# Optimization experiments

Hardware: AMD Instinct MI355X
Metric: run time of the kernel (lower is better)

## Reference

```python
import jax, jax.numpy as jnp
import numpy as np

BN_EPS = 1e-5


def cond_conv(x, att_w, att_b, weight, pad):
    """CondConv: per-sample expert-mixed conv.
    x: [N,C,H,W]; att_w: [K,C]; att_b: [K]; weight: [K,O,I,kh,kw]; pad: (ph,pw)."""
    pooled = x.mean(axis=(2, 3))                         # [N,C]  (AdaptiveAvgPool2d(1))
    att = jax.nn.sigmoid(pooled @ att_w.T + att_b)       # [N,K]  (1x1 conv + sigmoid)
    agg_w = jnp.einsum('nk,koihw->noihw', att, weight)   # per-sample kernels [N,O,I,kh,kw]

    def conv1(xi, wi):
        return jax.lax.conv_general_dilated(
            xi[None], wi, window_strides=(1, 1),
            padding=[(pad[0], pad[0]), (pad[1], pad[1])],
            dimension_numbers=('NCHW', 'OIHW', 'NCHW'))[0]

    return jax.vmap(conv1)(x, agg_w)                     # [N,O,H,W]


def batchnorm(x, gamma, beta):
    # training-mode BN: biased batch stats over (N,H,W)
    mean = x.mean(axis=(0, 2, 3), keepdims=True)
    var = x.var(axis=(0, 2, 3), keepdims=True)
    xn = (x - mean) * jax.lax.rsqrt(var + BN_EPS)
    return xn * gamma[None, :, None, None] + beta[None, :, None, None]


def channel_shuffle(x, g):
    N, C, H, W = x.shape
    return x.reshape(N, g, C // g, H, W).transpose(0, 2, 1, 3, 4).reshape(N, C, H, W)


def setup_inputs() -> dict:
    key = jax.random.key(0)
    ks = jax.random.split(key, 8)
    N, C, H, W = 32, 256, 64, 64
    Cb, K = C // 4, 4
    inp = {
        'x': jax.random.normal(ks[0], (N, C, H, W), jnp.float32),
        'sq_att_w': jax.random.normal(ks[1], (K, Cb), jnp.float32) * 0.1,
        'sq_att_b': jnp.zeros((K,), jnp.float32),
        'sq_w': jax.random.normal(ks[2], (K, Cb, Cb, 3, 3), jnp.float32) * 0.05,
        'sq_g': jnp.ones((Cb,), jnp.float32),
        'sq_b': jnp.zeros((Cb,), jnp.float32),
        'ver_att_w': jax.random.normal(ks[3], (K, Cb), jnp.float32) * 0.1,
        'ver_att_b': jnp.zeros((K,), jnp.float32),
        'ver_w': jax.random.normal(ks[4], (K, Cb, Cb, 3, 1), jnp.float32) * 0.05,
        'ver_g': jnp.ones((Cb,), jnp.float32),
        'ver_b': jnp.zeros((Cb,), jnp.float32),
        'hor_att_w': jax.random.normal(ks[5], (K, Cb), jnp.float32) * 0.1,
        'hor_att_b': jnp.zeros((K,), jnp.float32),
        'hor_w': jax.random.normal(ks[6], (K, Cb, Cb, 1, 3), jnp.float32) * 0.05,
        'hor_g': jnp.ones((Cb,), jnp.float32),
        'hor_b': jnp.zeros((Cb,), jnp.float32),
    }
    return inp


def reference(x, sq_att_w, sq_att_b, sq_w, sq_g, sq_b,
              ver_att_w, ver_att_b, ver_w, ver_g, ver_b,
              hor_att_w, hor_att_b, hor_w, hor_g, hor_b):
    # q_Split: chunk into 4 along channels
    s0, s1, s2, s3 = jnp.split(x, 4, axis=1)
    # square branch: CondConv 3x3 pad 1 + BN
    sq = batchnorm(cond_conv(s1, sq_att_w, sq_att_b, sq_w, (1, 1)), sq_g, sq_b)
    # vertical branch: CondConv 3x1 pad (1,0) + BN (crop layer is Identity since offset=0)
    ve = batchnorm(cond_conv(s2, ver_att_w, ver_att_b, ver_w, (1, 0)), ver_g, ver_b)
    # horizontal branch: CondConv 1x3 pad (0,1) + BN
    ho = batchnorm(cond_conv(s3, hor_att_w, hor_att_b, hor_w, (0, 1)), hor_g, hor_b)
    out = jnp.concatenate((s0, sq, ve, ho), axis=1)
    return channel_shuffle(out, 8)
```

## Files before the change

### kernel.cpp

```cpp
#include <hip/hip_runtime.h>
#include <cstddef>
#include <cstdint>


typedef __attribute__((ext_vector_type(8))) short frag8;
typedef __attribute__((ext_vector_type(16))) float accf16;

#define HW 4096
#define CNT_INV (1.0f / 131072.0f)
#define CSTR 1056
#define RSTR 8448
#define XT_BR (32ull * 66 * 8448)

#define WS_POOLED 0
#define WS_SS     24576
#define WS_PST    24960
#define WS_WBF_SQ  221568
#define WS_WBF_VER 811392
#define WS_WBF_HOR 1008000
#define WS_XT      1204608
#define WS_CVOUT   14586240

__device__ __forceinline__ int shuf_ch(int c) { return ((c & 31) << 3) | (c >> 5); }

__device__ __forceinline__ unsigned bf16pair(float a, float b) {
    unsigned ua = __builtin_bit_cast(unsigned, a);
    unsigned ub = __builtin_bit_cast(unsigned, b);
    ua = (ua + 0x7fffu + ((ua >> 16) & 1u)) >> 16;
    ub = (ub + 0x7fffu + ((ub >> 16) & 1u)) >> 16;
    return ua | (ub << 16);
}

__device__ __forceinline__ unsigned short bf16r(float a) {
    unsigned ua = __builtin_bit_cast(unsigned, a);
    return (unsigned short)((ua + 0x7fffu + ((ua >> 16) & 1u)) >> 16);
}

__device__ __forceinline__ float bf16lo(unsigned u) {
    return __builtin_bit_cast(float, u << 16);
}
__device__ __forceinline__ float bf16hi(unsigned u) {
    return __builtin_bit_cast(float, u & 0xffff0000u);
}

__device__ __forceinline__ void gload_lds16(const void* g, void* l) {
    __builtin_amdgcn_global_load_lds(
        (const __attribute__((address_space(1))) void*)g,
        (__attribute__((address_space(3))) void*)l, 16, 0, 0);
}

__global__ void __launch_bounds__(256) prepass_kernel(
    const float* __restrict__ x, unsigned char* __restrict__ xt,
    float* __restrict__ pooled4) {
    const int bid = blockIdx.x;
    const int hq = bid & 3;
    const int c8 = (bid >> 2) & 7;
    const int n = (bid >> 5) & 31;
    const int b = bid >> 10;
    const int tid = threadIdx.x;
    const int w = tid & 63, q = tid >> 6;
    const float* xb = x + (size_t)(n * 256 + 64 * (b + 1) + c8 * 8) * HW;
    unsigned char* xtb = xt + (size_t)b * XT_BR + (size_t)n * 66 * RSTR + c8 * CSTR;

    float ps[8] = {0.f, 0.f, 0.f, 0.f, 0.f, 0.f, 0.f, 0.f};
#pragma unroll
    for (int it = 0; it < 4; ++it) {
        const int h = hq * 16 + it * 4 + q;
        float v[8];
#pragma unroll
        for (int j = 0; j < 8; ++j) v[j] = xb[(size_t)j * HW + h * 64 + w];
        unsigned pk[4];
#pragma unroll
        for (int j = 0; j < 4; ++j) pk[j] = bf16pair(v[2 * j], v[2 * j + 1]);
        *(uint4*)(xtb + (size_t)(h + 1) * RSTR + (w + 1) * 16) = *(uint4*)pk;
#pragma unroll
        for (int j = 0; j < 8; ++j) ps[j] += v[j];
    }
    if (hq == 0) {
        for (int idx = tid; idx < 260; idx += 256) {
            int p, slot;
            if (idx < 66)       { p = 0;         slot = idx; }
            else if (idx < 132) { p = 65;        slot = idx - 66; }
            else if (idx < 196) { p = idx - 131; slot = 0; }
            else                { p = idx - 195; slot = 65; }
            *(uint4*)(xtb + (size_t)p * RSTR + slot * 16) = uint4{0, 0, 0, 0};
        }
    }
    __shared__ float red[4][8];
#pragma unroll
    for (int j = 0; j < 8; ++j)
#pragma unroll
        for (int off = 32; off; off >>= 1) ps[j] += __shfl_down(ps[j], off, 64);
    if ((tid & 63) == 0)
#pragma unroll
        for (int j = 0; j < 8; ++j) red[q][j] = ps[j];
    __syncthreads();
    if (tid < 8)
        pooled4[hq * 6144 + (b * 32 + n) * 64 + c8 * 8 + tid] =
            red[0][tid] + red[1][tid] + red[2][tid] + red[3][tid];
}

template <int TAPS>
__device__ __forceinline__ void aggbf_body(const float* __restrict__ w,
                                           const float* __restrict__ pooled_b,
                                           const float* __restrict__ aw,
                                           const float* __restrict__ ab,
                                           unsigned* __restrict__ wbf, int bid) {
    const int tid = threadIdx.x;
    int idx = bid * 256 + tid;
    int ip = idx & 31;
    int o  = (idx >> 5) & 63;
    int t  = (idx >> 11) % TAPS;
    int n  = (idx >> 11) / TAPS;

    __shared__ float satt[4];
    if (tid < 64) {
        const int base = n * 64 + tid;
        float p = (pooled_b[base] + pooled_b[base + 6144] +
                   pooled_b[base + 12288] + pooled_b[base + 18432]) *
                  (1.f / 4096.f);
#pragma unroll
        for (int k = 0; k < 4; ++k) {
            float v = p * aw[k * 64 + tid];
#pragma unroll
            for (int off = 32; off; off >>= 1) v += __shfl_down(v, off, 64);
            if (tid == 0) satt[k] = 1.f / (1.f + expf(-(v + ab[k])));
        }
    }
    __syncthreads();
    const float a0 = satt[0], a1 = satt[1], a2 = satt[2], a3 = satt[3];

    constexpr int PS = 64 * 64 * TAPS;
    int base = (o * 64 + ip * 2) * TAPS + t;
    float v0 = a0*w[base] + a1*w[PS+base] + a2*w[2*PS+base] + a3*w[3*PS+base];
    int base1 = base + TAPS;
    float v1 = a0*w[base1] + a1*w[PS+base1] + a2*w[2*PS+base1] + a3*w[3*PS+base1];
    int f = ip >> 2, jj = ip & 3;
    wbf[(((n * TAPS + t) * 8 + f) * 64 + o) * 4 + jj] = bf16pair(v0, v1);
}

__global__ void __launch_bounds__(256) aggbf_all_kernel(
    const float* __restrict__ pooled,
    const float* __restrict__ aw0, const float* __restrict__ ab0,
    const float* __restrict__ aw1, const float* __restrict__ ab1,
    const float* __restrict__ aw2, const float* __restrict__ ab2,
    const float* __restrict__ sq_w, const float* __restrict__ ver_w,
    const float* __restrict__ hor_w,
    unsigned* __restrict__ wsq, unsigned* __restrict__ wver,
    unsigned* __restrict__ whor) {
    int bid = blockIdx.x;
    if (bid < 2304)
        aggbf_body<9>(sq_w, pooled, aw0, ab0, wsq, bid);
    else if (bid < 3072)
        aggbf_body<3>(ver_w, pooled + 2048, aw1, ab1, wver, bid - 2304);
    else
        aggbf_body<3>(hor_w, pooled + 4096, aw2, ab2, whor, bid - 3072);
}

#define LOADA(dst, tt) \
    _Pragma("unroll") for (int kk = 0; kk < 4; ++kk) { \
        dst[kk]     = wp[(tt) * 512 + kk * 128]; \
        dst[4 + kk] = wp[(tt) * 512 + kk * 128 + 32]; \
    }

#define TAPSTEP(tt, CUR) { \
    const int r_ = (tt) / KW, dw_ = (tt) % KW - PW; \
    const unsigned char* bp_ = xs + (rh * 2 + r_) * RSTR + hi * CSTR + \
                               (wcol + dw_ + 1) * 16; \
    _Pragma("unroll") for (int kk = 0; kk < 4; ++kk) { \
        frag8 b0 = *(const frag8*)(bp_ + kk * 2 * CSTR); \
        frag8 b1 = *(const frag8*)(bp_ + kk * 2 * CSTR + RSTR); \
        a00 = __builtin_amdgcn_mfma_f32_32x32x16_bf16(CUR[kk],     b0, a00, 0, 0, 0); \
        a10 = __builtin_amdgcn_mfma_f32_32x32x16_bf16(CUR[4 + kk], b0, a10, 0, 0, 0); \
        a01 = __builtin_amdgcn_mfma_f32_32x32x16_bf16(CUR[kk],     b1, a01, 0, 0, 0); \
        a11 = __builtin_amdgcn_mfma_f32_32x32x16_bf16(CUR[4 + kk], b1, a11, 0, 0, 0); \
    } }

template <int KH, int KW, int PH, int PW>
__device__ __forceinline__ void conv_body(
    const unsigned char* __restrict__ xt, const unsigned* __restrict__ wbf,
    unsigned short* __restrict__ cvout, float* __restrict__ pst, int cbase,
    int bid, unsigned char* xs, float (*red1)[2][2][16],
    float (*red2)[2][2][16]) {
    constexpr int TAPS = KH * KW;
    constexpr int HB = 4;
    constexpr int ROWS = HB + KH - 1;
    constexpr int TOT = ROWS * RSTR;
    constexpr int NCH = (TOT + 1023) >> 10;
    const int hb = bid & 15, n = bid >> 4;
    const int h0 = hb * HB;
    const int tid = threadIdx.x;
    const int lane = tid & 63;
    const int wv = tid >> 6;
    const int rh = wv >> 1, wn = wv & 1;
    const int l31 = lane & 31, hi = lane >> 5;
    const int wcol = wn * 32 + l31;

    {
        const unsigned char* src = xt +
            (size_t)(n * 66 + h0 + (KH == 1 ? 1 : 0)) * RSTR + lane * 16;
#pragma unroll
        for (int c = wv; c < NCH; c += 4)
            gload_lds16(src + (c << 10), xs + (c << 10));
    }

    const frag8* wp = (const frag8*)wbf + (size_t)n * TAPS * 512 + hi * 64 + l31;

    frag8 aA[8], aB[8];
    LOADA(aA, 0);
    __syncthreads();

    accf16 a00 = {}, a01 = {}, a10 = {}, a11 = {};
#pragma unroll
    for (int t = 0; t < TAPS; t += 2) {
        if (t + 1 < TAPS) LOADA(aB, t + 1);
        TAPSTEP(t, aA);
        if (t + 2 < TAPS) LOADA(aA, t + 2);
        if (t + 1 < TAPS) TAPSTEP(t + 1, aB);
    }

    {
        unsigned short* cb = cvout + (size_t)(n * 192 + (cbase - 64)) * HW +
                             (h0 + rh * 2) * 64 + wcol;
#pragma unroll
        for (int rg = 0; rg < 16; ++rg) {
            const int o = (rg & 3) + 8 * (rg >> 2) + 4 * hi;
            unsigned short* p0 = cb + (size_t)o * HW;
            p0[0]  = bf16r(a00[rg]);
            p0[64] = bf16r(a01[rg]);
            unsigned short* p1 = cb + (size_t)(o + 32) * HW;
            p1[0]  = bf16r(a10[rg]);
            p1[64] = bf16r(a11[rg]);
        }
    }

#pragma unroll
    for (int rg = 0; rg < 16; ++rg) {
        float u1 = a00[rg] + a01[rg];
        float u2 = a00[rg] * a00[rg] + a01[rg] * a01[rg];
        float w1 = a10[rg] + a11[rg];
        float w2 = a10[rg] * a10[rg] + a11[rg] * a11[rg];
#pragma unroll
        for (int off = 16; off; off >>= 1) {
            u1 += __shfl_down(u1, off, 32);
            u2 += __shfl_down(u2, off, 32);
            w1 += __shfl_down(w1, off, 32);
            w2 += __shfl_down(w2, off, 32);
        }
        if (l31 == 0) {
            red1[wv][0][hi][rg] = u1; red2[wv][0][hi][rg] = u2;
            red1[wv][1][hi][rg] = w1; red2[wv][1][hi][rg] = w2;
        }
    }
    __syncthreads();
    if (tid < 64) {
        const int rg = tid & 15, hi2 = (tid >> 4) & 1, wm2 = tid >> 5;
        float s1 = 0.f, s2 = 0.f;
#pragma unroll
        for (int v = 0; v < 4; ++v) {
            s1 += red1[v][wm2][hi2][rg];
            s2 += red2[v][wm2][hi2][rg];
        }
        const int o = wm2 * 32 + (rg & 3) + 8 * (rg >> 2) + 4 * hi2;
        const int slot = n * 16 + hb;
        pst[o * 1024 + slot] = s1;
        pst[o * 1024 + 512 + slot] = s2;
    }
}

__device__ __forceinline__ void s0_body(const float* __restrict__ x,
                                        float* __restrict__ out, int sid) {
    const int c8 = sid & 7, n = sid >> 3, tid = threadIdx.x;
#pragma unroll
    for (int j = 0; j < 8; ++j) {
        const int c = c8 * 8 + j;
        const float4* s = (const float4*)(x + (size_t)(n * 256 + c) * HW);
        float4* d = (float4*)(out + (size_t)(n * 256 + shuf_ch(c)) * HW);
#pragma unroll
        for (int it = 0; it < 4; ++it) d[tid + it * 256] = s[tid + it * 256];
    }
}

__global__ void __launch_bounds__(256, 3) conv_all_kernel(
    const float* __restrict__ x, const unsigned char* __restrict__ xt,
    const unsigned* __restrict__ wsq, const unsigned* __restrict__ wver,
    const unsigned* __restrict__ whor,
    unsigned short* __restrict__ cvout, float* __restrict__ pst,
    float* __restrict__ out) {
    __shared__ __align__(16) unsigned char xs[6 * RSTR + 512];
    __shared__ float red1[4][2][2][16], red2[4][2][2][16];
    int raw = blockIdx.x;
    if (raw >= 1536) { s0_body(x, out, raw - 1536); return; }
    int bid = (raw & 7) * 192 + (raw >> 3);
    if (bid < 512)
        conv_body<3, 3, 1, 1>(xt, wsq, cvout, pst, 64, bid, xs, red1, red2);
    else if (bid < 1024)
        conv_body<3, 1, 1, 0>(xt + XT_BR, wver, cvout, pst + 65536, 128,
                              bid - 512, xs, red1, red2);
    else
        conv_body<1, 3, 0, 1>(xt + 2 * XT_BR, whor, cvout, pst + 131072, 192,
                              bid - 1024, xs, red1, red2);
}

__global__ void __launch_bounds__(256) bnstats_all_kernel(
    const float* __restrict__ pst,
    const float* __restrict__ g0, const float* __restrict__ b0,
    const float* __restrict__ g1, const float* __restrict__ b1,
    const float* __restrict__ g2, const float* __restrict__ b2,
    float* __restrict__ ss) {
    int br = blockIdx.x >> 6, o = blockIdx.x & 63, t = threadIdx.x;
    const float* gamma = (br == 0) ? g0 : (br == 1) ? g1 : g2;
    const float* beta  = (br == 0) ? b0 : (br == 1) ? b1 : b2;
    const float* p = pst + br * 65536 + o * 1024;
    float s1 = 0.f, s2 = 0.f;
    for (int i = t; i < 512; i += 256) {
        s1 += p[i];
        s2 += p[512 + i];
    }
#pragma unroll
    for (int off = 32; off; off >>= 1) {
        s1 += __shfl_down(s1, off, 64);
        s2 += __shfl_down(s2, off, 64);
    }
    __shared__ float r1[4], r2[4];
    if ((t & 63) == 0) { r1[t >> 6] = s1; r2[t >> 6] = s2; }
    __syncthreads();
    if (t == 0) {
        float S1 = r1[0] + r1[1] + r1[2] + r1[3];
        float S2 = r2[0] + r2[1] + r2[2] + r2[3];
        float mean = S1 * CNT_INV;
        float var = S2 * CNT_INV - mean * mean;
        float scale = rsqrtf(var + 1e-5f) * gamma[o];
        ss[br * 128 + o * 2 + 0] = scale;
        ss[br * 128 + o * 2 + 1] = beta[o] - mean * scale;
    }
}

__global__ void __launch_bounds__(256) bn_all_kernel(
    const unsigned short* __restrict__ cvout, float* __restrict__ out,
    const float* __restrict__ ss) {
    int g = blockIdx.x;
    int half = g & 1;
    int n = (g >> 1) & 31;
    int o = (g >> 6) & 63;
    int sub = g >> 12;
    float scale = ss[sub * 128 + o * 2], shift = ss[sub * 128 + o * 2 + 1];
    const uint4* src = (const uint4*)(cvout +
        (size_t)(n * 192 + sub * 64 + o) * HW + half * 2048) + threadIdx.x;
    float* dst = out + (size_t)(n * 256 + shuf_ch(64 * (sub + 1) + o)) * HW +
                 half * 2048 + threadIdx.x * 8;
    uint4 r = *src;
    float4 f0, f1;
    f0.x = fmaf(bf16lo(r.x), scale, shift);
    f0.y = fmaf(bf16hi(r.x), scale, shift);
    f0.z = fmaf(bf16lo(r.y), scale, shift);
    f0.w = fmaf(bf16hi(r.y), scale, shift);
    f1.x = fmaf(bf16lo(r.z), scale, shift);
    f1.y = fmaf(bf16hi(r.z), scale, shift);
    f1.z = fmaf(bf16lo(r.w), scale, shift);
    f1.w = fmaf(bf16hi(r.w), scale, shift);
    *(float4*)dst = f0;
    *(float4*)(dst + 4) = f1;
}

extern "C" void kernel_launch(void* const* d_in, const int* in_sizes, int n_in,
                              void* d_out, int out_size, void* d_ws, size_t ws_size,
                              hipStream_t stream) {
    const float* x        = (const float*)d_in[0];
    const float* sq_att_w = (const float*)d_in[1];
    const float* sq_att_b = (const float*)d_in[2];
    const float* sq_w     = (const float*)d_in[3];
    const float* sq_g     = (const float*)d_in[4];
    const float* sq_b     = (const float*)d_in[5];
    const float* ver_att_w= (const float*)d_in[6];
    const float* ver_att_b= (const float*)d_in[7];
    const float* ver_w    = (const float*)d_in[8];
    const float* ver_g    = (const float*)d_in[9];
    const float* ver_b    = (const float*)d_in[10];
    const float* hor_att_w= (const float*)d_in[11];
    const float* hor_att_b= (const float*)d_in[12];
    const float* hor_w    = (const float*)d_in[13];
    const float* hor_g    = (const float*)d_in[14];
    const float* hor_b    = (const float*)d_in[15];
    float* out = (float*)d_out;
    float* ws = (float*)d_ws;

    float* pooled = ws + WS_POOLED;
    float* ss     = ws + WS_SS;
    float* pst    = ws + WS_PST;
    unsigned* wbf_sq  = (unsigned*)(ws + WS_WBF_SQ);
    unsigned* wbf_ver = (unsigned*)(ws + WS_WBF_VER);
    unsigned* wbf_hor = (unsigned*)(ws + WS_WBF_HOR);
    unsigned char* xt = (unsigned char*)(ws + WS_XT);
    unsigned short* cvout = (unsigned short*)(ws + WS_CVOUT);

    prepass_kernel<<<3072, 256, 0, stream>>>(x, xt, pooled);
    aggbf_all_kernel<<<3840, 256, 0, stream>>>(pooled,
                                               sq_att_w, sq_att_b,
                                               ver_att_w, ver_att_b,
                                               hor_att_w, hor_att_b,
                                               sq_w, ver_w, hor_w,
                                               wbf_sq, wbf_ver, wbf_hor);
    conv_all_kernel<<<1792, 256, 0, stream>>>(x, xt, wbf_sq, wbf_ver, wbf_hor,
                                              cvout, pst, out);
    bnstats_all_kernel<<<192, 256, 0, stream>>>(pst, sq_g, sq_b, ver_g, ver_b,
                                                hor_g, hor_b, ss);
    bn_all_kernel<<<12288, 256, 0, stream>>>(cvout, out, ss);
}
```

Before: 144.0 us.

## Use 512-thread conv blocks with one row per wave and triple-buffered weight loads

The conv kernel now runs 8 waves per block, each computing a single output row with two accumulators instead of four, which halves accumulator register pressure and raises the launch-bounds occupancy target. Weight fragments are triple-buffered across taps, and the BN partial-sum reduction reuses the input LDS buffer after an extra barrier instead of separate shared arrays. The copy-through s0 path packs two former blocks into one 512-thread block, shrinking the grid. The cost is less B-fragment reuse per A load and an added synchronization.

```diff
diff --git a/kernel.cpp b/kernel.cpp
--- a/kernel.cpp
+++ b/kernel.cpp
@@ -69,10 +69,10 @@
         float v[8];
 #pragma unroll
         for (int j = 0; j < 8; ++j) v[j] = xb[(size_t)j * HW + h * 64 + w];
-        unsigned pk[4];
-#pragma unroll
-        for (int j = 0; j < 4; ++j) pk[j] = bf16pair(v[2 * j], v[2 * j + 1]);
-        *(uint4*)(xtb + (size_t)(h + 1) * RSTR + (w + 1) * 16) = *(uint4*)pk;
+        unsigned pkk[4];
+#pragma unroll
+        for (int j = 0; j < 4; ++j) pkk[j] = bf16pair(v[2 * j], v[2 * j + 1]);
+        *(uint4*)(xtb + (size_t)(h + 1) * RSTR + (w + 1) * 16) = *(uint4*)pkk;
 #pragma unroll
         for (int j = 0; j < 8; ++j) ps[j] += v[j];
     }
@@ -165,34 +165,28 @@
 
 #define TAPSTEP(tt, CUR) { \
     const int r_ = (tt) / KW, dw_ = (tt) % KW - PW; \
-    const unsigned char* bp_ = xs + (rh * 2 + r_) * RSTR + hi * CSTR + \
+    const unsigned char* bp_ = xs + (rw + r_) * RSTR + hi * CSTR + \
                                (wcol + dw_ + 1) * 16; \
     _Pragma("unroll") for (int kk = 0; kk < 4; ++kk) { \
         frag8 b0 = *(const frag8*)(bp_ + kk * 2 * CSTR); \
-        frag8 b1 = *(const frag8*)(bp_ + kk * 2 * CSTR + RSTR); \
-        a00 = __builtin_amdgcn_mfma_f32_32x32x16_bf16(CUR[kk],     b0, a00, 0, 0, 0); \
-        a10 = __builtin_amdgcn_mfma_f32_32x32x16_bf16(CUR[4 + kk], b0, a10, 0, 0, 0); \
-        a01 = __builtin_amdgcn_mfma_f32_32x32x16_bf16(CUR[kk],     b1, a01, 0, 0, 0); \
-        a11 = __builtin_amdgcn_mfma_f32_32x32x16_bf16(CUR[4 + kk], b1, a11, 0, 0, 0); \
+        ac0 = __builtin_amdgcn_mfma_f32_32x32x16_bf16(CUR[kk],     b0, ac0, 0, 0, 0); \
+        ac1 = __builtin_amdgcn_mfma_f32_32x32x16_bf16(CUR[4 + kk], b0, ac1, 0, 0, 0); \
     } }
 
 template <int KH, int KW, int PH, int PW>
 __device__ __forceinline__ void conv_body(
     const unsigned char* __restrict__ xt, const unsigned* __restrict__ wbf,
     unsigned short* __restrict__ cvout, float* __restrict__ pst, int cbase,
-    int bid, unsigned char* xs, float (*red1)[2][2][16],
-    float (*red2)[2][2][16]) {
+    int bid, unsigned char* xs) {
     constexpr int TAPS = KH * KW;
     constexpr int HB = 4;
     constexpr int ROWS = HB + KH - 1;
-    constexpr int TOT = ROWS * RSTR;
-    constexpr int NCH = (TOT + 1023) >> 10;
+    constexpr int NCH = (ROWS * RSTR + 1023) >> 10;
     const int hb = bid & 15, n = bid >> 4;
     const int h0 = hb * HB;
     const int tid = threadIdx.x;
-    const int lane = tid & 63;
-    const int wv = tid >> 6;
-    const int rh = wv >> 1, wn = wv & 1;
+    const int lane = tid & 63, wv = tid >> 6;
+    const int rw = wv >> 1, wn = wv & 1;
     const int l31 = lane & 31, hi = lane >> 5;
     const int wcol = wn * 32 + l31;
 
@@ -200,46 +194,50 @@
         const unsigned char* src = xt +
             (size_t)(n * 66 + h0 + (KH == 1 ? 1 : 0)) * RSTR + lane * 16;
 #pragma unroll
-        for (int c = wv; c < NCH; c += 4)
+        for (int c = wv; c < NCH; c += 8)
             gload_lds16(src + (c << 10), xs + (c << 10));
     }
 
     const frag8* wp = (const frag8*)wbf + (size_t)n * TAPS * 512 + hi * 64 + l31;
-
-    frag8 aA[8], aB[8];
-    LOADA(aA, 0);
-    __syncthreads();
-
-    accf16 a00 = {}, a01 = {}, a10 = {}, a11 = {};
-#pragma unroll
-    for (int t = 0; t < TAPS; t += 2) {
-        if (t + 1 < TAPS) LOADA(aB, t + 1);
-        TAPSTEP(t, aA);
-        if (t + 2 < TAPS) LOADA(aA, t + 2);
-        if (t + 1 < TAPS) TAPSTEP(t + 1, aB);
+    frag8 A0[8], A1[8], A2[8];
+    LOADA(A0, 0);
+    if (TAPS > 1) LOADA(A1, 1);
+    if (TAPS > 2) LOADA(A2, 2);
+    __syncthreads();
+
+    accf16 ac0 = {}, ac1 = {};
+#pragma unroll
+    for (int t = 0; t < TAPS; t += 3) {
+        TAPSTEP(t, A0);
+        if (t + 3 < TAPS) LOADA(A0, t + 3);
+        if (t + 1 < TAPS) {
+            TAPSTEP(t + 1, A1);
+            if (t + 4 < TAPS) LOADA(A1, t + 4);
+        }
+        if (t + 2 < TAPS) {
+            TAPSTEP(t + 2, A2);
+            if (t + 5 < TAPS) LOADA(A2, t + 5);
+        }
     }
 
     {
         unsigned short* cb = cvout + (size_t)(n * 192 + (cbase - 64)) * HW +
-                             (h0 + rh * 2) * 64 + wcol;
+                             (h0 + rw) * 64 + wcol;
 #pragma unroll
         for (int rg = 0; rg < 16; ++rg) {
             const int o = (rg & 3) + 8 * (rg >> 2) + 4 * hi;
-            unsigned short* p0 = cb + (size_t)o * HW;
-            p0[0]  = bf16r(a00[rg]);
-            p0[64] = bf16r(a01[rg]);
-            unsigned short* p1 = cb + (size_t)(o + 32) * HW;
-            p1[0]  = bf16r(a10[rg]);
-            p1[64] = bf16r(a11[rg]);
-        }
-    }
-
+            cb[(size_t)o * HW]        = bf16r(ac0[rg]);
+            cb[(size_t)(o + 32) * HW] = bf16r(ac1[rg]);
+        }
+    }
+
+    __syncthreads();
+    float* rsum = (float*)xs;
+    float* rsq  = rsum + 512;
 #pragma unroll
     for (int rg = 0; rg < 16; ++rg) {
-        float u1 = a00[rg] + a01[rg];
-        float u2 = a00[rg] * a00[rg] + a01[rg] * a01[rg];
-        float w1 = a10[rg] + a11[rg];
-        float w2 = a10[rg] * a10[rg] + a11[rg] * a11[rg];
+        float u1 = ac0[rg], u2 = ac0[rg] * ac0[rg];
+        float w1 = ac1[rg], w2 = ac1[rg] * ac1[rg];
 #pragma unroll
         for (int off = 16; off; off >>= 1) {
             u1 += __shfl_down(u1, off, 32);
@@ -248,8 +246,10 @@
             w2 += __shfl_down(w2, off, 32);
         }
         if (l31 == 0) {
-            red1[wv][0][hi][rg] = u1; red2[wv][0][hi][rg] = u2;
-            red1[wv][1][hi][rg] = w1; red2[wv][1][hi][rg] = w2;
+            rsum[((0 * 8 + wv) * 2 + hi) * 16 + rg] = u1;
+            rsq [((0 * 8 + wv) * 2 + hi) * 16 + rg] = u2;
+            rsum[((1 * 8 + wv) * 2 + hi) * 16 + rg] = w1;
+            rsq [((1 * 8 + wv) * 2 + hi) * 16 + rg] = w2;
         }
     }
     __syncthreads();
@@ -257,9 +257,9 @@
         const int rg = tid & 15, hi2 = (tid >> 4) & 1, wm2 = tid >> 5;
         float s1 = 0.f, s2 = 0.f;
 #pragma unroll
-        for (int v = 0; v < 4; ++v) {
-            s1 += red1[v][wm2][hi2][rg];
-            s2 += red2[v][wm2][hi2][rg];
+        for (int v = 0; v < 8; ++v) {
+            s1 += rsum[((wm2 * 8 + v) * 2 + hi2) * 16 + rg];
+            s2 += rsq [((wm2 * 8 + v) * 2 + hi2) * 16 + rg];
         }
         const int o = wm2 * 32 + (rg & 3) + 8 * (rg >> 2) + 4 * hi2;
         const int slot = n * 16 + hb;
@@ -268,38 +268,40 @@
     }
 }
 
-__device__ __forceinline__ void s0_body(const float* __restrict__ x,
-                                        float* __restrict__ out, int sid) {
-    const int c8 = sid & 7, n = sid >> 3, tid = threadIdx.x;
+__device__ __forceinline__ void s0_body512(const float* __restrict__ x,
+                                           float* __restrict__ out, int bid) {
+    const int tid = threadIdx.x;
+    const int sid = bid * 2 + (tid >> 8);
+    const int t = tid & 255;
+    const int c8 = sid & 7, n = sid >> 3;
 #pragma unroll
     for (int j = 0; j < 8; ++j) {
         const int c = c8 * 8 + j;
         const float4* s = (const float4*)(x + (size_t)(n * 256 + c) * HW);
         float4* d = (float4*)(out + (size_t)(n * 256 + shuf_ch(c)) * HW);
 #pragma unroll
-        for (int it = 0; it < 4; ++it) d[tid + it * 256] = s[tid + it * 256];
-    }
-}
-
-__global__ void __launch_bounds__(256, 3) conv_all_kernel(
+        for (int it = 0; it < 4; ++it) d[t + it * 256] = s[t + it * 256];
+    }
+}
+
+__global__ void __launch_bounds__(512, 6) conv_all_kernel(
     const float* __restrict__ x, const unsigned char* __restrict__ xt,
     const unsigned* __restrict__ wsq, const unsigned* __restrict__ wver,
     const unsigned* __restrict__ whor,
     unsigned short* __restrict__ cvout, float* __restrict__ pst,
     float* __restrict__ out) {
     __shared__ __align__(16) unsigned char xs[6 * RSTR + 512];
-    __shared__ float red1[4][2][2][16], red2[4][2][2][16];
     int raw = blockIdx.x;
-    if (raw >= 1536) { s0_body(x, out, raw - 1536); return; }
+    if (raw >= 1536) { s0_body512(x, out, raw - 1536); return; }
     int bid = (raw & 7) * 192 + (raw >> 3);
     if (bid < 512)
-        conv_body<3, 3, 1, 1>(xt, wsq, cvout, pst, 64, bid, xs, red1, red2);
+        conv_body<3, 3, 1, 1>(xt, wsq, cvout, pst, 64, bid, xs);
     else if (bid < 1024)
         conv_body<3, 1, 1, 0>(xt + XT_BR, wver, cvout, pst + 65536, 128,
-                              bid - 512, xs, red1, red2);
+                              bid - 512, xs);
     else
         conv_body<1, 3, 0, 1>(xt + 2 * XT_BR, whor, cvout, pst + 131072, 192,
-                              bid - 1024, xs, red1, red2);
+                              bid - 1024, xs);
 }
 
 __global__ void __launch_bounds__(256) bnstats_all_kernel(
@@ -401,7 +403,7 @@
                                                hor_att_w, hor_att_b,
                                                sq_w, ver_w, hor_w,
                                                wbf_sq, wbf_ver, wbf_hor);
-    conv_all_kernel<<<1792, 256, 0, stream>>>(x, xt, wbf_sq, wbf_ver, wbf_hor,
+    conv_all_kernel<<<1664, 512, 0, stream>>>(x, xt, wbf_sq, wbf_ver, wbf_hor,
                                               cvout, pst, out);
     bnstats_all_kernel<<<192, 256, 0, stream>>>(pst, sq_g, sq_b, ver_g, ver_b,
                                                 hor_g, hor_b, ss);
```

Result: slower. 212.9 us (+47.8%).
